# Performance work log

Hardware: AMD Instinct MI355X
Metric: run time of the kernel (lower is better)

## Reference

```python
import jax, jax.numpy as jnp
import numpy as np

# Multi-scale feature pyramid (H, W) per level, standard Deformable-DETR for ~800x800 input
SHAPES = [(100, 100), (50, 50), (25, 25), (13, 13)]
D = 256      # d_model
NH = 8       # n_heads
NL = 4       # n_levels
NP = 4       # n_points
HD = D // NH # head_dim = 32
B = 2
S = sum(h * w for h, w in SHAPES)  # 13294
Lq = S  # encoder-style: one query per multi-scale token


def setup_inputs() -> dict:
    key = jax.random.key(0)
    ks = jax.random.split(key, 11)
    return {
        "query": jax.random.normal(ks[0], (B, Lq, D), jnp.float32),
        "reference_points": jax.random.uniform(ks[1], (B, Lq, NL, 2), jnp.float32),
        "value": jax.random.normal(ks[2], (B, S, D), jnp.float32),
        "W_val": jax.random.normal(ks[3], (D, D), jnp.float32) * 0.02,
        "b_val": jnp.zeros((D,), jnp.float32),
        "W_off": jax.random.normal(ks[4], (D, NH * NL * NP * 2), jnp.float32) * 0.01,
        "b_off": jax.random.normal(ks[5], (NH * NL * NP * 2,), jnp.float32) * 0.5,
        "W_attn": jax.random.normal(ks[6], (D, NH * NL * NP), jnp.float32) * 0.02,
        "b_attn": jnp.zeros((NH * NL * NP,), jnp.float32),
        "W_out": jax.random.normal(ks[7], (D, D), jnp.float32) * 0.02,
        "b_out": jnp.zeros((D,), jnp.float32),
    }


def _bilinear_sample(valf, x, y, H, W):
    """grid_sample(mode=bilinear, padding_mode=zeros, align_corners=False).
    valf: [N, H*W, C] flattened feature map; x, y: [N, P] pixel-space coords
    (already converted via x = loc_x*W - 0.5). Returns [N, P, C].
    """
    x0 = jnp.floor(x); y0 = jnp.floor(y)
    x1 = x0 + 1.0;     y1 = y0 + 1.0
    wx1 = x - x0; wx0 = 1.0 - wx1
    wy1 = y - y0; wy0 = 1.0 - wy1

    def corner(xi, yi, w):
        inb = (xi >= 0) & (xi <= W - 1) & (yi >= 0) & (yi <= H - 1)
        xi_c = jnp.clip(xi, 0, W - 1).astype(jnp.int32)
        yi_c = jnp.clip(yi, 0, H - 1).astype(jnp.int32)
        idx = yi_c * W + xi_c                                   # [N, P]
        v = jnp.take_along_axis(valf, idx[..., None], axis=1)   # [N, P, C]
        return v * (w * inb.astype(valf.dtype))[..., None]

    return (corner(x0, y0, wx0 * wy0) + corner(x1, y0, wx1 * wy0)
            + corner(x0, y1, wx0 * wy1) + corner(x1, y1, wx1 * wy1))


def reference(query, reference_points, value, W_val, b_val, W_off, b_off,
              W_attn, b_attn, W_out, b_out):
    Bq, L, _ = query.shape
    # value projection, split into heads: [B, S, NH, HD]
    val = (value @ W_val + b_val).reshape(Bq, S, NH, HD)
    # sampling offsets and attention weights from query
    offsets = (query @ W_off + b_off).reshape(Bq, L, NH, NL, NP, 2)
    w = (query @ W_attn + b_attn).reshape(Bq, L, NH, NL * NP)
    w = jax.nn.softmax(w, axis=-1).reshape(Bq, L, NH, NL, NP)
    # normalize offsets by (W, H) per level; 2D reference points path
    offset_norm = jnp.array([[wd, h] for h, wd in SHAPES], jnp.float32)  # [NL, 2]
    locs = (reference_points[:, :, None, :, None, :]
            + offsets / offset_norm[None, None, None, :, None, :])       # [B,L,NH,NL,NP,2]

    splits = [h * wd for h, wd in SHAPES]
    starts = np.concatenate([[0], np.cumsum(splits)])
    out_acc = jnp.zeros((Bq, L, NH, HD), query.dtype)
    for lvl, (H, W) in enumerate(SHAPES):
        vl = val[:, starts[lvl]:starts[lvl + 1]]                 # [B, HW, NH, HD]
        vl = vl.transpose(0, 2, 1, 3).reshape(Bq * NH, H * W, HD)
        loc = locs[:, :, :, lvl].transpose(0, 2, 1, 3, 4).reshape(Bq * NH, L * NP, 2)
        x = loc[..., 0] * W - 0.5   # align_corners=False pixel coords
        y = loc[..., 1] * H - 0.5
        s = _bilinear_sample(vl, x, y, H, W).reshape(Bq, NH, L, NP, HD)
        wl = w[:, :, :, lvl].transpose(0, 2, 1, 3)               # [B, NH, L, NP]
        out_acc = out_acc + jnp.einsum('bhqpd,bhqp->bqhd', s, wl)
    out = out_acc.reshape(Bq, L, NH * HD)
    return out @ W_out + b_out
```

## Files before the change

kernel.cpp:

```cpp
#include <hip/hip_runtime.h>
#include <hip/hip_bf16.h>
#include <math.h>

#define B_    2
#define NH_   8
#define NL_   4
#define NP_   4
#define HD_   32
#define S_    13294
#define L_    13294
#define M_    26588

__device__ __constant__ int c_H[NL_]     = {100, 50, 25, 13};
__device__ __constant__ int c_W[NL_]     = {100, 50, 25, 13};
__device__ __constant__ int c_start[NL_] = {0, 10000, 12500, 13125};

typedef __attribute__((ext_vector_type(8))) short  short8;
typedef __attribute__((ext_vector_type(4))) float  float4v;

__device__ __forceinline__ unsigned short f2bf(float f) {
    unsigned u = __float_as_uint(f);
    unsigned r = 0x7fffu + ((u >> 16) & 1u);
    return (unsigned short)((u + r) >> 16);
}
__device__ __forceinline__ unsigned short f2h(float f) {
    _Float16 h = (_Float16)f;
    return __builtin_bit_cast(unsigned short, h);
}
__device__ __forceinline__ float h2f(unsigned short u) {
    _Float16 h = __builtin_bit_cast(_Float16, u);
    return (float)h;
}

__global__ __launch_bounds__(256) void prep_weights(
    const float* __restrict__ W_val, const float* __restrict__ W_off,
    const float* __restrict__ W_attn, const float* __restrict__ b_off,
    const float* __restrict__ b_attn, const float* __restrict__ W_out,
    unsigned short* __restrict__ wt_val, unsigned short* __restrict__ wt_oa,
    unsigned short* __restrict__ wt_out, float* __restrict__ bias_oa)
{
    int i = blockIdx.x * 256 + threadIdx.x;
    if (i < 65536) {
        int n = i >> 8, k = i & 255;
        wt_val[i] = f2bf(W_val[k * 256 + n]);
    } else if (i < 65536 + 98304) {
        int j = i - 65536;
        int n = j >> 8, k = j & 255;
        float v = (n < 256) ? W_off[k * 256 + n] : W_attn[k * 128 + (n - 256)];
        wt_oa[j] = f2bf(v);
    } else if (i < 65536 + 98304 + 65536) {
        int j = i - 163840;
        int n = j >> 8, k = j & 255;
        wt_out[j] = f2bf(W_out[k * 256 + n]);
    } else if (i < 229376 + 384) {
        int j = i - 229376;
        bias_oa[j] = (j < 256) ? b_off[j] : b_attn[j - 256];
    }
}

template<int N, int OUT, bool AF32>
__device__ __forceinline__ void gemm_body(
    const void* __restrict__ Av,
    const unsigned short* __restrict__ WT,
    const float* __restrict__ bias,
    void* __restrict__ Cv,
    unsigned short (* __restrict__ As)[40],
    unsigned short (* __restrict__ Bs)[40])
{
    constexpr int NT  = N / 64;
    constexpr int NCH = N / 64;

    const int tid  = threadIdx.x;
    const int lane = tid & 63;
    const int wave = tid >> 6;
    const int rowBase = blockIdx.x * 64;
    const int wcol = wave * (N / 4);

    const int ar   = tid >> 2;
    const int ako  = (tid & 3) * 8;
    const int grow = rowBase + ar;

    float4v acc[4][NT] = {};
    float4 pa0, pa1;
    short8 pah;
    short8 pb[NCH];

    auto loadAB = [&](int k0) {
        if constexpr (AF32) {
            const float* A = (const float*)Av;
            if (grow < M_) {
                pa0 = *reinterpret_cast<const float4*>(A + (size_t)grow * 256 + k0 + ako);
                pa1 = *reinterpret_cast<const float4*>(A + (size_t)grow * 256 + k0 + ako + 4);
            } else {
                pa0 = make_float4(0.f, 0.f, 0.f, 0.f); pa1 = pa0;
            }
        } else {
            const unsigned short* A = (const unsigned short*)Av;
            if (grow < M_)
                pah = *reinterpret_cast<const short8*>(A + (size_t)grow * 256 + k0 + ako);
            else
                pah = short8{};
        }
#pragma unroll
        for (int i = 0; i < NCH; ++i) {
            const int c = tid + i * 256;
            pb[i] = *reinterpret_cast<const short8*>(
                WT + (size_t)(c >> 2) * 256 + k0 + (c & 3) * 8);
        }
    };

    auto storeLDS = [&]() {
        short8 s;
        if constexpr (AF32) {
            s[0] = (short)f2bf(pa0.x); s[1] = (short)f2bf(pa0.y);
            s[2] = (short)f2bf(pa0.z); s[3] = (short)f2bf(pa0.w);
            s[4] = (short)f2bf(pa1.x); s[5] = (short)f2bf(pa1.y);
            s[6] = (short)f2bf(pa1.z); s[7] = (short)f2bf(pa1.w);
        } else {
            s = pah;
        }
        *reinterpret_cast<short8*>(&As[ar][ako]) = s;
#pragma unroll
        for (int i = 0; i < NCH; ++i) {
            const int c = tid + i * 256;
            *reinterpret_cast<short8*>(&Bs[c >> 2][(c & 3) * 8]) = pb[i];
        }
    };

    const int fr = lane & 15;
    const int fk = (lane >> 4) * 8;

    loadAB(0);
#pragma unroll
    for (int it = 0; it < 8; ++it) {
        __syncthreads();
        storeLDS();
        __syncthreads();
        if (it < 7) loadAB((it + 1) * 32);

        short8 af[4], bf[NT];
#pragma unroll
        for (int t = 0; t < 4; ++t)
            af[t] = *reinterpret_cast<const short8*>(&As[t * 16 + fr][fk]);
#pragma unroll
        for (int t = 0; t < NT; ++t)
            bf[t] = *reinterpret_cast<const short8*>(&Bs[wcol + t * 16 + fr][fk]);
#pragma unroll
        for (int mt = 0; mt < 4; ++mt)
#pragma unroll
            for (int nt = 0; nt < NT; ++nt)
                acc[mt][nt] = __builtin_amdgcn_mfma_f32_16x16x32_bf16(
                    af[mt], bf[nt], acc[mt][nt], 0, 0, 0);
    }

    const int dn  = lane & 15;
    const int dm0 = (lane >> 4) * 4;
#pragma unroll
    for (int mt = 0; mt < 4; ++mt) {
#pragma unroll
        for (int nt = 0; nt < NT; ++nt) {
            const int col = wcol + nt * 16 + dn;
            const float bv = bias[col];
#pragma unroll
            for (int r = 0; r < 4; ++r) {
                const int row = rowBase + mt * 16 + dm0 + r;
                if (row < M_) {
                    const float v = acc[mt][nt][r] + bv;
                    if constexpr (OUT == 0)
                        ((unsigned short*)Cv)[(size_t)row * 256 + col] = f2h(v);
                    else if constexpr (OUT == 1)
                        ((float*)Cv)[(size_t)row * 384 + col] = v;
                    else
                        ((float*)Cv)[(size_t)row * 256 + col] = v;
                }
            }
        }
    }
}

__global__ __launch_bounds__(256) void gemm_vq(
    const float* __restrict__ value, const float* __restrict__ query,
    const unsigned short* __restrict__ wt_val, const unsigned short* __restrict__ wt_oa,
    const float* __restrict__ b_val, const float* __restrict__ bias_oa,
    unsigned short* __restrict__ val_f16, float* __restrict__ oa_f)
{
    __shared__ unsigned short As[64][40];
    __shared__ unsigned short Bs[384][40];
    if (blockIdx.y == 0)
        gemm_body<256, 0, true>(value, wt_val, b_val, val_f16, As, Bs);
    else
        gemm_body<384, 1, true>(query, wt_oa, bias_oa, oa_f, As, Bs);
}

__global__ __launch_bounds__(256) void gemm_out2(
    const unsigned short* __restrict__ Abf,
    const unsigned short* __restrict__ WT,
    const float* __restrict__ bias, float* __restrict__ C)
{
    __shared__ unsigned short As[64][40];
    __shared__ unsigned short Bs[256][40];
    gemm_body<256, 2, false>(Abf, WT, bias, C, As, Bs);
}

__global__ __launch_bounds__(256) void deform_sample_v4(
    const unsigned short* __restrict__ val,
    const float* __restrict__ refp,
    const float* __restrict__ oa,
    unsigned short* __restrict__ acc)
{
    const int tid = threadIdx.x;
    const int q0  = blockIdx.x * 8;

    __shared__ float sLog[8][128];
    __shared__ float sMS[8][8][2];
    __shared__ int   sPack[8][4][16][8];

    {
        const int q  = tid >> 5;
        const int f  = tid & 31;
        const int bq = min(q0 + q, M_ - 1);
        float4 v = *reinterpret_cast<const float4*>(oa + (size_t)bq * 384 + 256 + f * 4);
        *reinterpret_cast<float4*>(&sLog[q][f * 4]) = v;
    }
    __syncthreads();

    if (tid < 64) {
        const int q = tid >> 3, h = tid & 7;
        float m = -1e30f;
#pragma unroll
        for (int i = 0; i < 16; ++i) m = fmaxf(m, sLog[q][h * 16 + i]);
        float s = 0.f;
#pragma unroll
        for (int i = 0; i < 16; ++i) s += __expf(sLog[q][h * 16 + i] - m);
        sMS[q][h][0] = m;
        sMS[q][h][1] = 1.f / s;
    }
    __syncthreads();

#pragma unroll
    for (int k = 0; k < 4; ++k) {
        const int e   = tid + k * 256;
        const int q   = e >> 7;
        const int t   = e & 127;
        const int h   = t >> 4;
        const int lp  = t & 15;
        const int lvl = lp >> 2;
        const int p   = lp & 3;
        const int bq  = min(q0 + q, M_ - 1);

        const float wgt = __expf(sLog[q][t] - sMS[q][h][0]) * sMS[q][h][1];

        const int Wi = c_W[lvl], Hi = c_H[lvl], st = c_start[lvl];
        const float rx = refp[((size_t)bq * NL_ + lvl) * 2 + 0];
        const float ry = refp[((size_t)bq * NL_ + lvl) * 2 + 1];
        const float ox = oa[(size_t)bq * 384 + h * 32 + lvl * 8 + p * 2 + 0];
        const float oy = oa[(size_t)bq * 384 + h * 32 + lvl * 8 + p * 2 + 1];
        const float x = rx * (float)Wi + ox - 0.5f;
        const float y = ry * (float)Hi + oy - 0.5f;

        const float x0f = floorf(x), y0f = floorf(y);
        const int   x0 = (int)x0f,   y0 = (int)y0f;
        const float wx1 = x - x0f, wx0 = 1.f - wx1;
        const float wy1 = y - y0f, wy0 = 1.f - wy1;

        const int   cx[4] = {x0, x0 + 1, x0,     x0 + 1};
        const int   cy[4] = {y0, y0,     y0 + 1, y0 + 1};
        const float cw[4] = {wx0 * wy0, wx1 * wy0, wx0 * wy1, wx1 * wy1};
#pragma unroll
        for (int c = 0; c < 4; ++c) {
            const bool inb = (cx[c] >= 0) & (cx[c] < Wi) & (cy[c] >= 0) & (cy[c] < Hi);
            const int xi = min(max(cx[c], 0), Wi - 1);
            const int yi = min(max(cy[c], 0), Hi - 1);
            const int idx = st + yi * Wi + xi;
            const unsigned short wh = f2h(inb ? wgt * cw[c] : 0.f);
            sPack[q][c][lp][h] = idx | ((int)wh << 16);
        }
    }
    __syncthreads();

    const int q  = tid >> 5;
    const int h  = (tid >> 2) & 7;
    const int d4 = tid & 3;
    const int bq = q0 + q;
    const int b  = min(bq, M_ - 1) / L_;
    const unsigned short* vb = val + (size_t)b * S_ * 256 + h * 32 + d4 * 8;

    float a0 = 0, a1 = 0, a2 = 0, a3 = 0, a4 = 0, a5 = 0, a6 = 0, a7 = 0;
#pragma unroll 8
    for (int i = 0; i < 64; ++i) {
        const int lp = i >> 2;
        const int c  = i & 3;
        const int pk = sPack[q][c][lp][h];
        const float w = h2f((unsigned short)((unsigned)pk >> 16));
        const unsigned idx = (unsigned)pk & 0xffffu;
        const int4 u = *reinterpret_cast<const int4*>(vb + (size_t)idx * 256);
        a0 += w * h2f((unsigned short)(u.x & 0xffff));
        a1 += w * h2f((unsigned short)((unsigned)u.x >> 16));
        a2 += w * h2f((unsigned short)(u.y & 0xffff));
        a3 += w * h2f((unsigned short)((unsigned)u.y >> 16));
        a4 += w * h2f((unsigned short)(u.z & 0xffff));
        a5 += w * h2f((unsigned short)((unsigned)u.z >> 16));
        a6 += w * h2f((unsigned short)(u.w & 0xffff));
        a7 += w * h2f((unsigned short)((unsigned)u.w >> 16));
    }
    if (bq < M_) {
        int4 o;
        o.x = (int)f2bf(a0) | ((int)f2bf(a1) << 16);
        o.y = (int)f2bf(a2) | ((int)f2bf(a3) << 16);
        o.z = (int)f2bf(a4) | ((int)f2bf(a5) << 16);
        o.w = (int)f2bf(a6) | ((int)f2bf(a7) << 16);
        *reinterpret_cast<int4*>(acc + (size_t)bq * 256 + h * 32 + d4 * 8) = o;
    }
}

extern "C" void kernel_launch(void* const* d_in, const int* in_sizes, int n_in,
                              void* d_out, int out_size, void* d_ws, size_t ws_size,
                              hipStream_t stream) {
    const float* query  = (const float*)d_in[0];
    const float* refp   = (const float*)d_in[1];
    const float* value  = (const float*)d_in[2];
    const float* W_val  = (const float*)d_in[3];
    const float* b_val  = (const float*)d_in[4];
    const float* W_off  = (const float*)d_in[5];
    const float* b_off  = (const float*)d_in[6];
    const float* W_attn = (const float*)d_in[7];
    const float* b_attn = (const float*)d_in[8];
    const float* W_out  = (const float*)d_in[9];
    const float* b_out  = (const float*)d_in[10];
    float* out = (float*)d_out;

    char* ws = (char*)d_ws;
    const size_t mb = (size_t)M_ * 256;
    unsigned short* val_f16 = (unsigned short*)ws;  ws += mb * 2;
    unsigned short* acc_bf  = (unsigned short*)ws;  ws += mb * 2;
    float*          oa_f    = (float*)ws;           ws += (size_t)M_ * 384 * 4;
    unsigned short* wt_val  = (unsigned short*)ws;  ws += 65536 * 2;
    unsigned short* wt_oa   = (unsigned short*)ws;  ws += 98304 * 2;
    unsigned short* wt_out  = (unsigned short*)ws;  ws += 65536 * 2;
    float*          bias_oa = (float*)ws;           ws += 384 * 4;

    dim3 blk(256);

    prep_weights<<<dim3(898), blk, 0, stream>>>(
        W_val, W_off, W_attn, b_off, b_attn, W_out, wt_val, wt_oa, wt_out, bias_oa);

    gemm_vq<<<dim3((M_ + 63) / 64, 2), blk, 0, stream>>>(
        value, query, wt_val, wt_oa, b_val, bias_oa, val_f16, oa_f);

    deform_sample_v4<<<dim3((M_ + 7) / 8), blk, 0, stream>>>(val_f16, refp, oa_f, acc_bf);

    gemm_out2<<<dim3((M_ + 63) / 64), blk, 0, stream>>>(acc_bf, wt_out, b_out, out);
}
```

Before: 207.6 us.

## Switch pipeline to fp16 with direct-register B loads and packed fp16 sampling

Moves all GEMMs from bf16 to fp16 MFMA and stores the offset/attention projection as fp16 instead of fp32, halving that intermediate's traffic. The GEMM now reads weight fragments straight from global memory into registers instead of staging them in LDS. It also double-buffers the A tile so only one barrier runs per k-step. The sampling kernel accumulates in packed fp16 (v_pk_fma style) rather than eight fp32 accumulators, which cuts ALU and conversion work. The cost is lower accuracy: fp16 accumulation over 64 weighted samples and fp16 offsets/logits may drift from the reference.

```diff
diff --git a/kernel.cpp b/kernel.cpp
--- a/kernel.cpp
+++ b/kernel.cpp
@@ -15,14 +15,10 @@
 __device__ __constant__ int c_W[NL_]     = {100, 50, 25, 13};
 __device__ __constant__ int c_start[NL_] = {0, 10000, 12500, 13125};
 
-typedef __attribute__((ext_vector_type(8))) short  short8;
-typedef __attribute__((ext_vector_type(4))) float  float4v;
-
-__device__ __forceinline__ unsigned short f2bf(float f) {
-    unsigned u = __float_as_uint(f);
-    unsigned r = 0x7fffu + ((u >> 16) & 1u);
-    return (unsigned short)((u + r) >> 16);
-}
+typedef __attribute__((ext_vector_type(8))) _Float16 f16x8;
+typedef __attribute__((ext_vector_type(2))) _Float16 f16x2;
+typedef __attribute__((ext_vector_type(4))) float    float4v;
+
 __device__ __forceinline__ unsigned short f2h(float f) {
     _Float16 h = (_Float16)f;
     return __builtin_bit_cast(unsigned short, h);
@@ -30,6 +26,9 @@
 __device__ __forceinline__ float h2f(unsigned short u) {
     _Float16 h = __builtin_bit_cast(_Float16, u);
     return (float)h;
+}
+__device__ __forceinline__ f16x2 pkrtz(float a, float b) {
+    return __builtin_bit_cast(f16x2, __builtin_amdgcn_cvt_pkrtz(a, b));
 }
 
 __global__ __launch_bounds__(256) void prep_weights(
@@ -42,16 +41,16 @@
     int i = blockIdx.x * 256 + threadIdx.x;
     if (i < 65536) {
         int n = i >> 8, k = i & 255;
-        wt_val[i] = f2bf(W_val[k * 256 + n]);
+        wt_val[i] = f2h(W_val[k * 256 + n]);
     } else if (i < 65536 + 98304) {
         int j = i - 65536;
         int n = j >> 8, k = j & 255;
         float v = (n < 256) ? W_off[k * 256 + n] : W_attn[k * 128 + (n - 256)];
-        wt_oa[j] = f2bf(v);
+        wt_oa[j] = f2h(v);
     } else if (i < 65536 + 98304 + 65536) {
         int j = i - 163840;
         int n = j >> 8, k = j & 255;
-        wt_out[j] = f2bf(W_out[k * 256 + n]);
+        wt_out[j] = f2h(W_out[k * 256 + n]);
     } else if (i < 229376 + 384) {
         int j = i - 229376;
         bias_oa[j] = (j < 256) ? b_off[j] : b_attn[j - 256];
@@ -64,11 +63,9 @@
     const unsigned short* __restrict__ WT,
     const float* __restrict__ bias,
     void* __restrict__ Cv,
-    unsigned short (* __restrict__ As)[40],
-    unsigned short (* __restrict__ Bs)[40])
-{
-    constexpr int NT  = N / 64;
-    constexpr int NCH = N / 64;
+    unsigned short (* __restrict__ As)[64][40])
+{
+    constexpr int NT = N / 64;
 
     const int tid  = threadIdx.x;
     const int lane = tid & 63;
@@ -79,78 +76,82 @@
     const int ar   = tid >> 2;
     const int ako  = (tid & 3) * 8;
     const int grow = rowBase + ar;
+    const int fr   = lane & 15;
+    const int fk   = (lane >> 4) * 8;
 
     float4v acc[4][NT] = {};
-    float4 pa0, pa1;
-    short8 pah;
-    short8 pb[NCH];
-
-    auto loadAB = [&](int k0) {
+
+    const unsigned short* bbase[NT];
+#pragma unroll
+    for (int t = 0; t < NT; ++t)
+        bbase[t] = WT + (size_t)(wcol + t * 16 + fr) * 256 + fk;
+
+    f16x8 curB[NT], nxtB[NT];
+    float4 ra0, ra1;
+    f16x8  rah;
+
+    auto loadA = [&](int k0) {
         if constexpr (AF32) {
             const float* A = (const float*)Av;
             if (grow < M_) {
-                pa0 = *reinterpret_cast<const float4*>(A + (size_t)grow * 256 + k0 + ako);
-                pa1 = *reinterpret_cast<const float4*>(A + (size_t)grow * 256 + k0 + ako + 4);
-            } else {
-                pa0 = make_float4(0.f, 0.f, 0.f, 0.f); pa1 = pa0;
-            }
+                ra0 = *reinterpret_cast<const float4*>(A + (size_t)grow * 256 + k0 + ako);
+                ra1 = *reinterpret_cast<const float4*>(A + (size_t)grow * 256 + k0 + ako + 4);
+            } else { ra0 = make_float4(0.f,0.f,0.f,0.f); ra1 = ra0; }
         } else {
             const unsigned short* A = (const unsigned short*)Av;
             if (grow < M_)
-                pah = *reinterpret_cast<const short8*>(A + (size_t)grow * 256 + k0 + ako);
+                rah = *reinterpret_cast<const f16x8*>(A + (size_t)grow * 256 + k0 + ako);
             else
-                pah = short8{};
-        }
-#pragma unroll
-        for (int i = 0; i < NCH; ++i) {
-            const int c = tid + i * 256;
-            pb[i] = *reinterpret_cast<const short8*>(
-                WT + (size_t)(c >> 2) * 256 + k0 + (c & 3) * 8);
+                rah = f16x8{};
         }
     };
-
-    auto storeLDS = [&]() {
-        short8 s;
+    auto storeA = [&](int buf) {
+        f16x8 s;
         if constexpr (AF32) {
-            s[0] = (short)f2bf(pa0.x); s[1] = (short)f2bf(pa0.y);
-            s[2] = (short)f2bf(pa0.z); s[3] = (short)f2bf(pa0.w);
-            s[4] = (short)f2bf(pa1.x); s[5] = (short)f2bf(pa1.y);
-            s[6] = (short)f2bf(pa1.z); s[7] = (short)f2bf(pa1.w);
+            f16x2 p0 = pkrtz(ra0.x, ra0.y);
+            f16x2 p1 = pkrtz(ra0.z, ra0.w);
+            f16x2 p2 = pkrtz(ra1.x, ra1.y);
+            f16x2 p3 = pkrtz(ra1.z, ra1.w);
+            s[0]=p0[0]; s[1]=p0[1]; s[2]=p1[0]; s[3]=p1[1];
+            s[4]=p2[0]; s[5]=p2[1]; s[6]=p3[0]; s[7]=p3[1];
         } else {
-            s = pah;
-        }
-        *reinterpret_cast<short8*>(&As[ar][ako]) = s;
-#pragma unroll
-        for (int i = 0; i < NCH; ++i) {
-            const int c = tid + i * 256;
-            *reinterpret_cast<short8*>(&Bs[c >> 2][(c & 3) * 8]) = pb[i];
-        }
+            s = rah;
+        }
+        *reinterpret_cast<f16x8*>(&As[buf][ar][ako]) = s;
     };
-
-    const int fr = lane & 15;
-    const int fk = (lane >> 4) * 8;
-
-    loadAB(0);
+    auto loadB = [&](f16x8* dst, int k0) {
+#pragma unroll
+        for (int t = 0; t < NT; ++t)
+            dst[t] = *reinterpret_cast<const f16x8*>(bbase[t] + k0);
+    };
+
+    loadA(0);
+    loadB(curB, 0);
+    storeA(0);
+    loadA(32);
+
 #pragma unroll
     for (int it = 0; it < 8; ++it) {
         __syncthreads();
-        storeLDS();
-        __syncthreads();
-        if (it < 7) loadAB((it + 1) * 32);
-
-        short8 af[4], bf[NT];
+        f16x8 af[4];
 #pragma unroll
         for (int t = 0; t < 4; ++t)
-            af[t] = *reinterpret_cast<const short8*>(&As[t * 16 + fr][fk]);
-#pragma unroll
-        for (int t = 0; t < NT; ++t)
-            bf[t] = *reinterpret_cast<const short8*>(&Bs[wcol + t * 16 + fr][fk]);
+            af[t] = *reinterpret_cast<const f16x8*>(&As[it & 1][t * 16 + fr][fk]);
+        if (it < 7) {
+            storeA((it + 1) & 1);
+            if (it < 6) loadA((it + 2) * 32);
+            loadB(nxtB, (it + 1) * 32);
+        }
 #pragma unroll
         for (int mt = 0; mt < 4; ++mt)
 #pragma unroll
             for (int nt = 0; nt < NT; ++nt)
-                acc[mt][nt] = __builtin_amdgcn_mfma_f32_16x16x32_bf16(
-                    af[mt], bf[nt], acc[mt][nt], 0, 0, 0);
+                acc[mt][nt] = __builtin_amdgcn_mfma_f32_16x16x32_f16(
+                    af[mt], curB[nt], acc[mt][nt], 0, 0, 0);
+        if (it < 7) {
+#pragma unroll
+            for (int t = 0; t < NT; ++t) curB[t] = nxtB[t];
+        }
     }
 
     const int dn  = lane & 15;
@@ -169,7 +170,7 @@
                     if constexpr (OUT == 0)
                         ((unsigned short*)Cv)[(size_t)row * 256 + col] = f2h(v);
                     else if constexpr (OUT == 1)
-                        ((float*)Cv)[(size_t)row * 384 + col] = v;
+                        ((unsigned short*)Cv)[(size_t)row * 384 + col] = f2h(v);
                     else
                         ((float*)Cv)[(size_t)row * 256 + col] = v;
                 }
@@ -182,36 +183,34 @@
     const float* __restrict__ value, const float* __restrict__ query,
     const unsigned short* __restrict__ wt_val, const unsigned short* __restrict__ wt_oa,
     const float* __restrict__ b_val, const float* __restrict__ bias_oa,
-    unsigned short* __restrict__ val_f16, float* __restrict__ oa_f)
-{
-    __shared__ unsigned short As[64][40];
-    __shared__ unsigned short Bs[384][40];
+    unsigned short* __restrict__ val_f16, unsigned short* __restrict__ oa_f16)
+{
+    __shared__ unsigned short As[2][64][40];
     if (blockIdx.y == 0)
-        gemm_body<256, 0, true>(value, wt_val, b_val, val_f16, As, Bs);
+        gemm_body<256, 0, true>(value, wt_val, b_val, val_f16, As);
     else
-        gemm_body<384, 1, true>(query, wt_oa, bias_oa, oa_f, As, Bs);
-}
-
-__global__ __launch_bounds__(256) void gemm_out2(
-    const unsigned short* __restrict__ Abf,
+        gemm_body<384, 1, true>(query, wt_oa, bias_oa, oa_f16, As);
+}
+
+__global__ __launch_bounds__(256) void gemm_out3(
+    const unsigned short* __restrict__ Af16,
     const unsigned short* __restrict__ WT,
     const float* __restrict__ bias, float* __restrict__ C)
 {
-    __shared__ unsigned short As[64][40];
-    __shared__ unsigned short Bs[256][40];
-    gemm_body<256, 2, false>(Abf, WT, bias, C, As, Bs);
-}
-
-__global__ __launch_bounds__(256) void deform_sample_v4(
+    __shared__ unsigned short As[2][64][40];
+    gemm_body<256, 2, false>(Af16, WT, bias, C, As);
+}
+
+__global__ __launch_bounds__(256) void deform_sample_v5(
     const unsigned short* __restrict__ val,
     const float* __restrict__ refp,
-    const float* __restrict__ oa,
+    const unsigned short* __restrict__ oa,
     unsigned short* __restrict__ acc)
 {
     const int tid = threadIdx.x;
     const int q0  = blockIdx.x * 8;
 
-    __shared__ float sLog[8][128];
+    __shared__ unsigned short sLog[8][128];
     __shared__ float sMS[8][8][2];
     __shared__ int   sPack[8][4][16][8];
 
@@ -219,8 +218,8 @@
         const int q  = tid >> 5;
         const int f  = tid & 31;
         const int bq = min(q0 + q, M_ - 1);
-        float4 v = *reinterpret_cast<const float4*>(oa + (size_t)bq * 384 + 256 + f * 4);
-        *reinterpret_cast<float4*>(&sLog[q][f * 4]) = v;
+        *reinterpret_cast<int2*>(&sLog[q][f * 4]) =
+            *reinterpret_cast<const int2*>(oa + (size_t)bq * 384 + 256 + f * 4);
     }
     __syncthreads();
 
@@ -228,10 +227,10 @@
         const int q = tid >> 3, h = tid & 7;
         float m = -1e30f;
 #pragma unroll
-        for (int i = 0; i < 16; ++i) m = fmaxf(m, sLog[q][h * 16 + i]);
+        for (int i = 0; i < 16; ++i) m = fmaxf(m, h2f(sLog[q][h * 16 + i]));
         float s = 0.f;
 #pragma unroll
-        for (int i = 0; i < 16; ++i) s += __expf(sLog[q][h * 16 + i] - m);
+        for (int i = 0; i < 16; ++i) s += __expf(h2f(sLog[q][h * 16 + i]) - m);
         sMS[q][h][0] = m;
         sMS[q][h][1] = 1.f / s;
     }
@@ -248,13 +247,13 @@
         const int p   = lp & 3;
         const int bq  = min(q0 + q, M_ - 1);
 
-        const float wgt = __expf(sLog[q][t] - sMS[q][h][0]) * sMS[q][h][1];
+        const float wgt = __expf(h2f(sLog[q][t]) - sMS[q][h][0]) * sMS[q][h][1];
 
         const int Wi = c_W[lvl], Hi = c_H[lvl], st = c_start[lvl];
         const float rx = refp[((size_t)bq * NL_ + lvl) * 2 + 0];
         const float ry = refp[((size_t)bq * NL_ + lvl) * 2 + 1];
-        const float ox = oa[(size_t)bq * 384 + h * 32 + lvl * 8 + p * 2 + 0];
-        const float oy = oa[(size_t)bq * 384 + h * 32 + lvl * 8 + p * 2 + 1];
+        const float ox = h2f(oa[(size_t)bq * 384 + h * 32 + lvl * 8 + p * 2 + 0]);
+        const float oy = h2f(oa[(size_t)bq * 384 + h * 32 + lvl * 8 + p * 2 + 1]);
         const float x = rx * (float)Wi + ox - 0.5f;
         const float y = ry * (float)Hi + oy - 0.5f;
 
@@ -285,30 +284,27 @@
     const int b  = min(bq, M_ - 1) / L_;
     const unsigned short* vb = val + (size_t)b * S_ * 256 + h * 32 + d4 * 8;
 
-    float a0 = 0, a1 = 0, a2 = 0, a3 = 0, a4 = 0, a5 = 0, a6 = 0, a7 = 0;
+    f16x2 A0{}, A1{}, A2{}, A3{};
 #pragma unroll 8
     for (int i = 0; i < 64; ++i) {
         const int lp = i >> 2;
         const int c  = i & 3;
         const int pk = sPack[q][c][lp][h];
-        const float w = h2f((unsigned short)((unsigned)pk >> 16));
-        const unsigned idx = (unsigned)pk & 0xffffu;
-        const int4 u = *reinterpret_cast<const int4*>(vb + (size_t)idx * 256);
-        a0 += w * h2f((unsigned short)(u.x & 0xffff));
-        a1 += w * h2f((unsigned short)((unsigned)u.x >> 16));
-        a2 += w * h2f((unsigned short)(u.y & 0xffff));
-        a3 += w * h2f((unsigned short)((unsigned)u.y >> 16));
-        a4 += w * h2f((unsigned short)(u.z & 0xffff));
-        a5 += w * h2f((unsigned short)((unsigned)u.z >> 16));
-        a6 += w * h2f((unsigned short)(u.w & 0xffff));
-        a7 += w * h2f((unsigned short)((unsigned)u.w >> 16));
+        const unsigned wb = (unsigned)pk >> 16;
+        const f16x2 w2 = __builtin_bit_cast(f16x2, (wb << 16) | wb);
+        const int4 u = *reinterpret_cast<const int4*>(
+            vb + (size_t)((unsigned)pk & 0xffffu) * 256);
+        A0 += w2 * __builtin_bit_cast(f16x2, u.x);
+        A1 += w2 * __builtin_bit_cast(f16x2, u.y);
+        A2 += w2 * __builtin_bit_cast(f16x2, u.z);
+        A3 += w2 * __builtin_bit_cast(f16x2, u.w);
     }
     if (bq < M_) {
         int4 o;
-        o.x = (int)f2bf(a0) | ((int)f2bf(a1) << 16);
-        o.y = (int)f2bf(a2) | ((int)f2bf(a3) << 16);
-        o.z = (int)f2bf(a4) | ((int)f2bf(a5) << 16);
-        o.w = (int)f2bf(a6) | ((int)f2bf(a7) << 16);
+        o.x = __builtin_bit_cast(int, A0);
+        o.y = __builtin_bit_cast(int, A1);
+        o.z = __builtin_bit_cast(int, A2);
+        o.w = __builtin_bit_cast(int, A3);
         *reinterpret_cast<int4*>(acc + (size_t)bq * 256 + h * 32 + d4 * 8) = o;
     }
 }
@@ -332,8 +328,8 @@
     char* ws = (char*)d_ws;
     const size_t mb = (size_t)M_ * 256;
     unsigned short* val_f16 = (unsigned short*)ws;  ws += mb * 2;
-    unsigned short* acc_bf  = (unsigned short*)ws;  ws += mb * 2;
-    float*          oa_f    = (float*)ws;           ws += (size_t)M_ * 384 * 4;
+    unsigned short* acc_f16 = (unsigned short*)ws;  ws += mb * 2;
+    unsigned short* oa_f16  = (unsigned short*)ws;  ws += (size_t)M_ * 384 * 2;
     unsigned short* wt_val  = (unsigned short*)ws;  ws += 65536 * 2;
     unsigned short* wt_oa   = (unsigned short*)ws;  ws += 98304 * 2;
     unsigned short* wt_out  = (unsigned short*)ws;  ws += 65536 * 2;
@@ -345,9 +341,9 @@
         W_val, W_off, W_attn, b_off, b_attn, W_out, wt_val, wt_oa, wt_out, bias_oa);
 
     gemm_vq<<<dim3((M_ + 63) / 64, 2), blk, 0, stream>>>(
-        value, query, wt_val, wt_oa, b_val, bias_oa, val_f16, oa_f);
-
-    deform_sample_v4<<<dim3((M_ + 7) / 8), blk, 0, stream>>>(val_f16, refp, oa_f, acc_bf);
-
-    gemm_out2<<<dim3((M_ + 63) / 64), blk, 0, stream>>>(acc_bf, wt_out, b_out, out);
-}
+        value, query, wt_val, wt_oa, b_val, bias_oa, val_f16, oa_f16);
+
+    deform_sample_v5<<<dim3((M_ + 7) / 8), blk, 0, stream>>>(val_f16, refp, oa_f16, acc_f16);
+
+    gemm_out3<<<dim3((M_ + 63) / 64), blk, 0, stream>>>(acc_f16, wt_out, b_out, out);
+}
```

Result: no change. 207.3 us (-0.2%).
